# Kernel tuning notes

Hardware: AMD Instinct MI355X
Metric: run time of the kernel (lower is better)

Reference implementation:

```python
import jax, jax.numpy as jnp
import numpy as np
from jax import lax

B, H, W = 10, 320, 1024
PTS, DENSE, WD, KMEAN = 500, 2000, 11, 10
N = B * PTS  # 5000 center rows


def setup_inputs() -> dict:
    key = jax.random.key(0)
    k1, k2, k3, k4, k5, k6 = jax.random.split(key, 6)
    disp = jax.random.uniform(k1, (B, 1, H, W), dtype=jnp.float32)
    # forepred is a binary foreground prediction map -> strong Sobel edges
    forepred = jnp.round(jax.random.uniform(k2, (B, 1, H, W), dtype=jnp.float32))
    centerx = jax.random.randint(k3, (N,), WD, W - WD, dtype=jnp.int32)
    centery = jax.random.randint(k4, (N,), WD, H - WD, dtype=jnp.int32)
    bx = jax.random.randint(k5, (N, DENSE), -WD, WD + 1, dtype=jnp.int32)
    by = jax.random.randint(k6, (N, DENSE), -7, 8, dtype=jnp.int32)
    return {"disp": disp, "forepred": forepred, "centerx": centerx,
            "centery": centery, "bx": bx, "by": by}


def _mask_grad(disp, forepred):
    # Sobel-x conv, padding=1, no bias
    wx = jnp.array([[-1., 0., 1.], [-2., 0., 2.], [-1., 0., 1.]],
                   dtype=forepred.dtype)[None, None]  # [1,1,3,3]
    g = lax.conv_general_dilated(forepred, wx, (1, 1), 'SAME')
    mg = jnp.abs(g)
    # 3x3 max-pool, stride 1, padding 1 ("expand")
    mg = lax.reduce_window(mg, -jnp.inf, lax.max, (1, 1, 3, 3), (1, 1, 1, 1), 'SAME')
    mg = mg * (disp > 0.007).astype(mg.dtype)
    mg = jnp.maximum(mg, 3.0) - 3.0  # clamp(min=3) - 3
    # zero 4-pixel borders (zeroArea = [0,1,2,3,-1,-2,-3,-4])
    zy = jnp.array([0, 1, 2, 3, H - 1, H - 2, H - 3, H - 4])
    zx = jnp.array([0, 1, 2, 3, W - 1, W - 2, W - 3, W - 4])
    mg = mg.at[:, :, zy, :].set(0.0)
    mg = mg.at[:, :, :, zx].set(0.0)
    return mg


def reference(disp, forepred, centerx, centery, bx, by):
    maskGrad = _mask_grad(disp, forepred)
    channelInd = jnp.repeat(jnp.arange(B, dtype=jnp.int32), PTS)  # [N]
    # on-border row validity (original compacts; we mask instead, jit-friendly)
    validRow = maskGrad[channelInd, 0, centery, centerx] > 0.1  # [N]

    sampledx = centerx[:, None] + bx  # [N, DENSE]
    sampledy = centery[:, None] + by
    flat = (channelInd[:, None].astype(jnp.int32) * H + sampledy) * W + sampledx
    sampledDisp = disp.reshape(-1)[flat]  # irregular gather, [N, DENSE]

    kmeanLarge = jnp.max(sampledDisp, axis=1, keepdims=True)
    kmeanSmall = jnp.min(sampledDisp, axis=1, keepdims=True)
    for _ in range(KMEAN):
        distLarge = jnp.abs(sampledDisp - kmeanLarge)
        distSmall = jnp.abs(sampledDisp - kmeanSmall)
        belongingLarge = (distLarge <= distSmall).astype(sampledDisp.dtype)
        belongingSmall = 1.0 - belongingLarge
        kmeanLarge = (jnp.sum(sampledDisp * belongingLarge, axis=1, keepdims=True)
                      / jnp.sum(belongingLarge, axis=1, keepdims=True))
        kmeanSmall = (jnp.sum(sampledDisp * belongingSmall, axis=1, keepdims=True)
                      / jnp.sum(belongingSmall, axis=1, keepdims=True))

    contrast = ((kmeanLarge - kmeanSmall)[:, 0] > 0.005) & \
               (jnp.sum(belongingLarge, axis=1) > 5)
    keep = (validRow & contrast).astype(sampledDisp.dtype)  # [N]
    # per-row [large, small] cluster means; rows failing selection zeroed
    out = jnp.concatenate([kmeanLarge, kmeanSmall], axis=1) * keep[:, None]
    return out
```

## Files before the change

kernel.cpp:

```cpp
#include <hip/hip_runtime.h>

namespace {

constexpr int Bn    = 10;
constexpr int H     = 320;
constexpr int W     = 1024;
constexpr int PTS   = 500;
constexpr int DENSE = 2000;
constexpr int N     = Bn * PTS;
constexpr int HWp   = H * W;
constexpr int ROWS_PER_BLOCK = 4;

__global__ __launch_bounds__(256, 4)
void rsbsp_kernel(const float* __restrict__ disp,
                  const float* __restrict__ forepred,
                  const int*   __restrict__ centerx,
                  const int*   __restrict__ centery,
                  const int*   __restrict__ bx,
                  const int*   __restrict__ by,
                  float*       __restrict__ out)
{
    const int wid  = threadIdx.x >> 6;
    const int lane = threadIdx.x & 63;
    const int row  = blockIdx.x * ROWS_PER_BLOCK + wid;
    const int b    = row / PTS;
    const int cx   = centerx[row];
    const int cy   = centery[row];
    const float* db = disp     + b * HWp;
    const float* fb = forepred + b * HWp;

    float F[5][5];
    #pragma unroll
    for (int a = 0; a < 5; ++a)
        #pragma unroll
        for (int c = 0; c < 5; ++c)
            F[a][c] = fb[(cy - 2 + a) * W + (cx - 2 + c)];

    float v = 0.f;
    #pragma unroll
    for (int dy = 0; dy < 3; ++dy)
        #pragma unroll
        for (int dx = 0; dx < 3; ++dx) {
            const float g = (F[dy    ][dx + 2] - F[dy    ][dx])
                    + 2.f * (F[dy + 1][dx + 2] - F[dy + 1][dx])
                    +       (F[dy + 2][dx + 2] - F[dy + 2][dx]);
            v = fmaxf(v, fabsf(g));
        }
    const float dcen = db[cy * W + cx];
    const float mgv  = fmaxf(v * ((dcen > 0.007f) ? 1.f : 0.f), 3.f) - 3.f;
    const bool validRow = mgv > 0.1f;

    const int4* bx4 = reinterpret_cast<const int4*>(bx + row * DENSE);
    const int4* by4 = reinterpret_cast<const int4*>(by + row * DENSE);
    const int cbase = cy * W + cx;

    float s[32];
    float mx = -INFINITY, mn = INFINITY, tot = 0.f;
    #pragma unroll
    for (int k = 0; k < 8; ++k) {
        const int q = lane + 64 * k;
        if (q < DENSE / 4) {
            const int4 xb = bx4[q];
            const int4 yb = by4[q];
            const float x0 = db[cbase + yb.x * W + xb.x];
            const float x1 = db[cbase + yb.y * W + xb.y];
            const float x2 = db[cbase + yb.z * W + xb.z];
            const float x3 = db[cbase + yb.w * W + xb.w];
            s[k * 4 + 0] = x0; s[k * 4 + 1] = x1;
            s[k * 4 + 2] = x2; s[k * 4 + 3] = x3;
            mx = fmaxf(fmaxf(fmaxf(mx, x0), fmaxf(x1, x2)), x3);
            mn = fminf(fminf(fminf(mn, x0), fminf(x1, x2)), x3);
            tot += (x0 + x1) + (x2 + x3);
        }
    }

    #pragma unroll
    for (int m = 1; m < 64; m <<= 1) {
        mx  = fmaxf(mx, __shfl_xor(mx, m));
        mn  = fminf(mn, __shfl_xor(mn, m));
        tot += __shfl_xor(tot, m);
    }

    float mL = mx, mS = mn;
    float cntL_last = 0.f;
    for (int it = 0; it < 10; ++it) {
        const float mid = 0.5f * (mL + mS);
        float sumL = 0.f;
        int   cnt  = 0;
        #pragma unroll
        for (int k = 0; k < 8; ++k) {
            const int q = lane + 64 * k;
            if (q < DENSE / 4) {
                #pragma unroll
                for (int r = 0; r < 4; ++r) {
                    const float x  = s[k * 4 + r];
                    const bool  bl = x >= mid;
                    sumL += bl ? x : 0.f;
                    cnt  += bl ? 1 : 0;
                }
            }
        }
        #pragma unroll
        for (int m = 1; m < 64; m <<= 1) {
            sumL += __shfl_xor(sumL, m);
            cnt  += __shfl_xor(cnt,  m);
        }
        const float cntL = (float)cnt;
        mL = sumL / cntL;
        mS = (tot - sumL) / ((float)DENSE - cntL);
        cntL_last = cntL;
    }

    if (lane == 0) {
        const bool contrast = ((mL - mS) > 0.005f) && (cntL_last > 5.f);
        const float keep = (validRow && contrast) ? 1.f : 0.f;
        out[row * 2 + 0] = mL * keep;
        out[row * 2 + 1] = mS * keep;
    }
}

}

extern "C" void kernel_launch(void* const* d_in, const int* in_sizes, int n_in,
                              void* d_out, int out_size, void* d_ws, size_t ws_size,
                              hipStream_t stream) {
    const float* disp = (const float*)d_in[0];
    const float* fore = (const float*)d_in[1];
    const int*   cx   = (const int*)d_in[2];
    const int*   cy   = (const int*)d_in[3];
    const int*   bxp  = (const int*)d_in[4];
    const int*   byp  = (const int*)d_in[5];
    float* out = (float*)d_out;

    rsbsp_kernel<<<N / ROWS_PER_BLOCK, 256, 0, stream>>>(disp, fore, cx, cy, bxp, byp, out);
}
```

Before: 136.8 us.

## Stage per-row disparity window in LDS and count cluster members via ballot

Each wave loads the 15x24 disparity window around its center into shared memory, and the 2000 irregular samples are gathered from LDS instead of global memory. The k-means loop now runs over all 32 register slots, with unused slots padded to -inf, and counts members with ballot+popcount instead of a per-lane counter shuffle reduction. Reciprocal approximations replace divisions in all but the final iteration, and launch bounds rise to 6 waves per SIMD. This trades global gather latency for LDS bank conflicts and a small window load. The approximate reciprocals could perturb the intermediate means slightly, and there is no barrier between the LDS stores and the reads, which relies on each wave only reading its own window.

```diff
diff --git a/kernel.cpp b/kernel.cpp
--- a/kernel.cpp
+++ b/kernel.cpp
@@ -9,9 +9,15 @@
 constexpr int DENSE = 2000;
 constexpr int N     = Bn * PTS;
 constexpr int HWp   = H * W;
-constexpr int ROWS_PER_BLOCK = 4;
+constexpr int RPB   = 4;
+constexpr int KITER = 10;
 
-__global__ __launch_bounds__(256, 4)
+constexpr int WY   = 15;
+constexpr int WX   = 24;
+constexpr int WSZ  = WY * WX;
+constexpr int WOFF = 7 * WX + 11;
+
+__global__ __launch_bounds__(256, 6)
 void rsbsp_kernel(const float* __restrict__ disp,
                   const float* __restrict__ forepred,
                   const int*   __restrict__ centerx,
@@ -20,14 +26,28 @@
                   const int*   __restrict__ by,
                   float*       __restrict__ out)
 {
+    __shared__ float win[RPB][WSZ];
+
     const int wid  = threadIdx.x >> 6;
     const int lane = threadIdx.x & 63;
-    const int row  = blockIdx.x * ROWS_PER_BLOCK + wid;
+    const int row  = blockIdx.x * RPB + wid;
     const int b    = row / PTS;
     const int cx   = centerx[row];
     const int cy   = centery[row];
     const float* db = disp     + b * HWp;
     const float* fb = forepred + b * HWp;
+
+    float* wl = win[wid];
+    const int gbase = (cy - 7) * W + (cx - 11);
+    #pragma unroll
+    for (int i = 0; i < 6; ++i) {
+        const unsigned w = (unsigned)(lane + 64 * i);
+        if (w < WSZ) {
+            const unsigned r = w / 24u;
+            const unsigned c = w - r * 24u;
+            wl[w] = db[gbase + r * W + c];
+        }
+    }
 
     float F[5][5];
     #pragma unroll
@@ -52,7 +72,6 @@
 
     const int4* bx4 = reinterpret_cast<const int4*>(bx + row * DENSE);
     const int4* by4 = reinterpret_cast<const int4*>(by + row * DENSE);
-    const int cbase = cy * W + cx;
 
     float s[32];
     float mx = -INFINITY, mn = INFINITY, tot = 0.f;
@@ -62,15 +81,18 @@
         if (q < DENSE / 4) {
             const int4 xb = bx4[q];
             const int4 yb = by4[q];
-            const float x0 = db[cbase + yb.x * W + xb.x];
-            const float x1 = db[cbase + yb.y * W + xb.y];
-            const float x2 = db[cbase + yb.z * W + xb.z];
-            const float x3 = db[cbase + yb.w * W + xb.w];
+            const float x0 = wl[yb.x * WX + xb.x + WOFF];
+            const float x1 = wl[yb.y * WX + xb.y + WOFF];
+            const float x2 = wl[yb.z * WX + xb.z + WOFF];
+            const float x3 = wl[yb.w * WX + xb.w + WOFF];
             s[k * 4 + 0] = x0; s[k * 4 + 1] = x1;
             s[k * 4 + 2] = x2; s[k * 4 + 3] = x3;
             mx = fmaxf(fmaxf(fmaxf(mx, x0), fmaxf(x1, x2)), x3);
             mn = fminf(fminf(fminf(mn, x0), fminf(x1, x2)), x3);
             tot += (x0 + x1) + (x2 + x3);
+        } else {
+            s[k * 4 + 0] = -INFINITY; s[k * 4 + 1] = -INFINITY;
+            s[k * 4 + 2] = -INFINITY; s[k * 4 + 3] = -INFINITY;
         }
     }
 
@@ -82,37 +104,36 @@
     }
 
     float mL = mx, mS = mn;
-    float cntL_last = 0.f;
-    for (int it = 0; it < 10; ++it) {
+    int cntLast = 0;
+    for (int it = 0; it < KITER; ++it) {
         const float mid = 0.5f * (mL + mS);
         float sumL = 0.f;
         int   cnt  = 0;
         #pragma unroll
-        for (int k = 0; k < 8; ++k) {
-            const int q = lane + 64 * k;
-            if (q < DENSE / 4) {
-                #pragma unroll
-                for (int r = 0; r < 4; ++r) {
-                    const float x  = s[k * 4 + r];
-                    const bool  bl = x >= mid;
-                    sumL += bl ? x : 0.f;
-                    cnt  += bl ? 1 : 0;
-                }
-            }
+        for (int j = 0; j < 32; ++j) {
+            const float x  = s[j];
+            const bool  bl = x >= mid;
+            sumL += bl ? x : 0.f;
+            cnt  += (int)__popcll(__ballot(bl));
         }
         #pragma unroll
-        for (int m = 1; m < 64; m <<= 1) {
-            sumL += __shfl_xor(sumL, m);
-            cnt  += __shfl_xor(cnt,  m);
+        for (int m = 1; m < 64; m <<= 1) sumL += __shfl_xor(sumL, m);
+
+        const float cf = (float)cnt;
+        const float df = (float)DENSE - cf;
+        if (it < KITER - 1) {
+            mL = sumL * __builtin_amdgcn_rcpf(cf);
+            mS = (tot - sumL) * __builtin_amdgcn_rcpf(df);
+        } else {
+            mL = sumL / cf;
+            mS = (tot - sumL) / df;
         }
-        const float cntL = (float)cnt;
-        mL = sumL / cntL;
-        mS = (tot - sumL) / ((float)DENSE - cntL);
-        cntL_last = cntL;
+        if (cnt == DENSE) mS = __int_as_float(0x7fc00000);
+        cntLast = cnt;
     }
 
     if (lane == 0) {
-        const bool contrast = ((mL - mS) > 0.005f) && (cntL_last > 5.f);
+        const bool contrast = ((mL - mS) > 0.005f) && (cntLast > 5);
         const float keep = (validRow && contrast) ? 1.f : 0.f;
         out[row * 2 + 0] = mL * keep;
         out[row * 2 + 1] = mS * keep;
@@ -132,5 +153,5 @@
     const int*   byp  = (const int*)d_in[5];
     float* out = (float*)d_out;
 
-    rsbsp_kernel<<<N / ROWS_PER_BLOCK, 256, 0, stream>>>(disp, fore, cx, cy, bxp, byp, out);
+    rsbsp_kernel<<<N / RPB, 256, 0, stream>>>(disp, fore, cx, cy, bxp, byp, out);
 }
```

New measurement: 136.3 us. No clear change (-0.4%).
